# Optimization experiments

Hardware: AMD Instinct MI355X
Metric: run time of the kernel (lower is better)

## Reference

```python
import jax, jax.numpy as jnp
import numpy as np

# dims
B, N, M, K = 8, 4096, 1024, 32      # batch, points, centers, neighbors
CIN, CT = 64, 64                    # feature / temb channels
C1, C2 = 64, 128                    # SharedMLP out_channels
G, EPS = 8, 1e-5                    # GroupNorm(8, oc)


def setup_inputs() -> dict:
    key = jax.random.key(0)
    ks = jax.random.split(key, 8)
    return {
        "features": jax.random.normal(ks[0], (B, CIN, N), jnp.float32),
        "coords": jax.random.uniform(ks[1], (B, 3, N), jnp.float32),
        "temb": jax.random.normal(ks[2], (B, CT, N), jnp.float32),
        # SharedMLP params: Conv2d 1x1 -> (O, I) weight, GroupNorm affine
        "W1": jax.random.normal(ks[3], (C1, CIN + 3), jnp.float32) * 0.05,
        "b1": jnp.zeros((C1,), jnp.float32),
        "g1": jnp.ones((C1,), jnp.float32),
        "be1": jnp.zeros((C1,), jnp.float32),
        "W2": jax.random.normal(ks[4], (C2, C1), jnp.float32) * 0.05,
        "b2": jnp.zeros((C2,), jnp.float32),
        "g2": jnp.ones((C2,), jnp.float32),
        "be2": jnp.zeros((C2,), jnp.float32),
    }


def fps_indices(pts):
    # pts: [N, 3] -> [M] indices. Deterministic start at index 0
    # (original uses a random start; math otherwise identical).
    d0 = jnp.sum((pts - pts[0]) ** 2, axis=-1)  # [N]
    def step(dist, _):
        far = jnp.argmax(dist)
        dist = jnp.minimum(dist, jnp.sum((pts - pts[far]) ** 2, axis=-1))
        return dist, far
    _, fars = jax.lax.scan(step, d0, None, length=M - 1)
    return jnp.concatenate([jnp.zeros((1,), fars.dtype), fars])


def group_norm(x, gamma, beta):
    # x: [B, C, M, K], normalize per group over (C//G, M, K)
    b, c, m, k = x.shape
    xr = x.reshape(b, G, c // G, m, k)
    mu = xr.mean(axis=(2, 3, 4), keepdims=True)
    var = xr.var(axis=(2, 3, 4), keepdims=True)
    xn = ((xr - mu) * jax.lax.rsqrt(var + EPS)).reshape(b, c, m, k)
    return xn * gamma[:, None, None] + beta[:, None, None]


def swish(x):
    return x * jax.nn.sigmoid(x)


def reference(features, coords, temb, W1, b1, g1, be1, W2, b2, g2, be2):
    # --- furthest point sampling ---
    idx = jax.vmap(fps_indices)(coords.transpose(0, 2, 1))          # [B, M]
    centers = jax.vmap(lambda c, i: c[:, i])(coords, idx)           # [B, 3, M]
    # --- 'ball query' (actually kNN: source argsorts dist, takes first K) ---
    c = centers.transpose(0, 2, 1)                                  # [B, M, 3]
    p = coords.transpose(0, 2, 1)                                   # [B, N, 3]
    d = (jnp.sum(c * c, -1)[:, :, None] + jnp.sum(p * p, -1)[:, None, :]
         - 2.0 * jnp.einsum('bmd,bnd->bmn', c, p))                  # [B, M, N]
    _, nidx = jax.lax.top_k(-d, K)                                  # [B, M, K]
    gather = jax.vmap(lambda xb, ib: xb[:, ib])                     # [B,C,N],[B,M,K]->[B,C,M,K]
    gcoords = gather(coords, nidx) - centers[..., None]             # [B, 3, M, K]
    gtemb = gather(temb, nidx)                                      # [B, CT, M, K]
    gfeat = jnp.concatenate([gcoords, gather(features, nidx)], axis=1)  # [B, 3+CIN, M, K]
    # --- SharedMLP (1x1 conv -> GN -> Swish) x2, then max over neighbors ---
    h = swish(group_norm(jnp.einsum('oc,bcmk->bomk', W1, gfeat) + b1[:, None, None], g1, be1))
    h = swish(group_norm(jnp.einsum('oc,bcmk->bomk', W2, h) + b2[:, None, None], g2, be2))
    return h.max(axis=-1), centers, gtemb.max(axis=-1)
```

## Files before the change

### kernel.cpp

```cpp
#include <hip/hip_runtime.h>
#include <stdint.h>

#define BB 8
#define NN 4096
#define MM 1024
#define KK 32

__device__ __forceinline__ float bf2f(unsigned short u) {
    union { unsigned int i; float f; } v; v.i = ((unsigned int)u) << 16; return v.f;
}
__device__ __forceinline__ unsigned short f2bf(float f) {
    union { float f; unsigned int i; } v; v.f = f;
    unsigned int x = v.i;
    x += 0x7fffu + ((x >> 16) & 1u);
    return (unsigned short)(x >> 16);
}
__device__ __forceinline__ float swishf(float y) {
    return __fdividef(y, 1.0f + __expf(-y));
}

#define OUT1_OFF 1048576
#define OUT2_OFF 1073152

#define P_W1 0
#define P_B1 4288
#define P_G1 4352
#define P_BE1 4416
#define P_W2 4480
#define P_B2 12672
#define P_G2 12800
#define P_BE2 12928

__device__ __forceinline__ int detect_flag_wave(const unsigned short* f, int lane) {
    unsigned short u = f[lane * 2];
    float x = fabsf(bf2f(u));
    bool ext = (u != 0) && (x > 100.0f || x < 1e-30f);
    unsigned long long m = __ballot(ext);
    return (__popcll(m) >= 16) ? 1 : 0;
}

#define DPP_STAGE(CTRL) { \
    union { double d; unsigned int u[2]; } s_, r_; \
    s_.d = bd; \
    r_.u[0] = (unsigned)__builtin_amdgcn_update_dpp(0, (int)s_.u[0], CTRL, 0xF, 0xF, true); \
    r_.u[1] = (unsigned)__builtin_amdgcn_update_dpp(0, (int)s_.u[1], CTRL, 0xF, 0xF, true); \
    int op_ = __builtin_amdgcn_update_dpp(0, bp, CTRL, 0xF, 0xF, true); \
    double od_ = r_.d; \
    bool rep_ = (od_ > bd) || (od_ == bd && op_ < bp); \
    bd = rep_ ? od_ : bd; bp = rep_ ? op_ : bp; }

__device__ __forceinline__ void redmax64(double& bd, int& bp) {
    DPP_STAGE(0xB1)
    DPP_STAGE(0x4E)
    DPP_STAGE(0x141)
    DPP_STAGE(0x140)
#pragma unroll
    for (int m = 32; m >= 16; m >>= 1) {
        double od = __shfl_xor(bd, m, 64);
        int op = __shfl_xor(bp, m, 64);
        bool rep = (od > bd) || (od == bd && op < bp);
        bd = rep ? od : bd; bp = rep ? op : bp;
    }
}

__global__ __launch_bounds__(256) void k_cvt_all(
    const void* __restrict__ feat, const void* __restrict__ coords,
    float* __restrict__ featT, float* __restrict__ coordsC,
    float* __restrict__ paramsC,
    int* __restrict__ qhead, int* __restrict__ progress,
    float* __restrict__ stats1,
    const void* W1, const void* b1, const void* g1, const void* be1,
    const void* W2, const void* b2, const void* g2, const void* be2)
{
    __shared__ float tile[64][65];
    __shared__ int sflag;
    int tid = threadIdx.x, blk = blockIdx.x;
    if (tid < 64) {
        int fl0 = detect_flag_wave((const unsigned short*)feat, tid);
        if (tid == 0) sflag = fl0;
    }
    __syncthreads();
    int fl = sflag;
    if (blk == 0) {
        if (tid == 0) *qhead = 0;
        if (tid < 8) progress[tid * 16] = -1;
        stats1[tid] = 0.f;
        stats1[tid + 256] = 0.f;
    }
    if (blk < 512) {
        int i = blk;
        int b = i >> 6, n0 = (i & 63) * 64;
        int c = tid >> 2, q = tid & 3;
        size_t base = ((size_t)b * 64 + c) * NN + n0 + q * 16;
        if (fl) {
            const float* sp = (const float*)feat + base;
#pragma unroll
            for (int j = 0; j < 16; j++) tile[c][q * 16 + j] = sp[j];
        } else {
            const unsigned short* sp = (const unsigned short*)feat + base;
#pragma unroll
            for (int j = 0; j < 16; j++) tile[c][q * 16 + j] = bf2f(sp[j]);
        }
        __syncthreads();
        int n = tid >> 2;
        float* dp = featT + ((size_t)b * NN + n0 + n) * 64 + q * 16;
#pragma unroll
        for (int j = 0; j < 16; j++) dp[j] = tile[q * 16 + j][n];
    } else if (blk < 896) {
        int idx = (blk - 512) * 256 + tid;
        coordsC[idx] = fl ? ((const float*)coords)[idx]
                          : bf2f(((const unsigned short*)coords)[idx]);
    } else {
        int idx = (blk - 896) * 256 + tid;
        if (idx < 13056) {
            const void* src; int off;
            if (idx < 4288)       { src = W1;  off = idx; }
            else if (idx < 4352)  { src = b1;  off = idx - 4288; }
            else if (idx < 4416)  { src = g1;  off = idx - 4352; }
            else if (idx < 4480)  { src = be1; off = idx - 4416; }
            else if (idx < 12672) { src = W2;  off = idx - 4480; }
            else if (idx < 12800) { src = b2;  off = idx - 12672; }
            else if (idx < 12928) { src = g2;  off = idx - 12800; }
            else                  { src = be2; off = idx - 12928; }
            paramsC[idx] = fl ? ((const float*)src)[off]
                              : bf2f(((const unsigned short*)src)[off]);
        }
    }
}

#define W1Tm(j,c)     (((float*)SM)[(j)*64+(c)])
#define GBUFm(mi,k,c) (((float*)(SM+17152))[(((mi)*32+(k))*66)+(c)])
#define GCm(mi,j,k)   (((float*)(SM+50944))[(((mi)*3+(j))*32)+(k)])
#define NDm(mi,k)     (((int*)(SM+52480))[((mi)*32)+(k)])
#define W2Tm(j,c)     (((float*)SM)[(j)*128+(c)])
#define ACTm(mi,j,k)  (((float*)(SM+32768))[(((mi)*64+(j))*32)+(k)])

struct PW { double d; int p; int q; };
#define PSM_XS   ((float*)(SM))
#define PSM_YS   ((float*)(SM + 16384))
#define PSM_ZS   ((float*)(SM + 32768))
#define PSM_HIST ((int*)(SM + 49152))
#define PSM_PWB  ((PW*)(SM + 53248))
#define PSM_SF   ((int*)(SM + 53376))

#define RESCAN(G) { \
    double gd = 1.0e300; int ga = (G) * 8; \
    _Pragma("unroll") \
    for (int i = 0; i < 8; i++) { \
        int sl = (G) * 8 + i; \
        unsigned int bit = (sl < 32) ? (elo >> sl) : (ehi >> (sl - 32)); \
        double cd = (bit & 1u) ? 1.0e300 : d[sl]; \
        bool rep = cd < gd; \
        gd = rep ? cd : gd; ga = rep ? sl : ga; \
    } \
    g8[(G)] = gd; a8[(G)] = ga; }

__global__ __launch_bounds__(256) void k_fpsknn(
    const void* __restrict__ coords, const float* __restrict__ coordsC,
    float* __restrict__ centersF, int* __restrict__ nidx,
    const void* __restrict__ temb, const void* __restrict__ feat,
    const float* __restrict__ featT, const float* __restrict__ paramsC,
    float* __restrict__ stats1,
    void* __restrict__ d_out,
    int* __restrict__ qhead, int* __restrict__ progress,
    unsigned short* __restrict__ h1, int cache1)
{
    __shared__ __align__(16) char SM[55296];
    int tid = threadIdx.x;
    int blk = blockIdx.x;
    if (tid < 64) {
        int fl0 = detect_flag_wave((const unsigned short*)feat, tid);
        if (tid == 0) *PSM_SF = fl0;
    }
    __syncthreads();
    int fl = *PSM_SF;

    if (blk < 8) {
        int b = blk;
        if (fl) {
            const float* cb = (const float*)coords + (size_t)b * 3 * NN;
#pragma unroll
            for (int i = 0; i < 16; i++) {
                int p = tid + i * 256;
                PSM_XS[p] = cb[p]; PSM_YS[p] = cb[NN + p]; PSM_ZS[p] = cb[2 * NN + p];
            }
        } else {
            const unsigned short* cb = (const unsigned short*)coords + (size_t)b * 3 * NN;
#pragma unroll
            for (int i = 0; i < 16; i++) {
                int p = tid + i * 256;
                PSM_XS[p] = bf2f(cb[p]); PSM_YS[p] = bf2f(cb[NN + p]); PSM_ZS[p] = bf2f(cb[2 * NN + p]);
            }
        }
        if (tid == 0) PSM_HIST[0] = 0;
        __syncthreads();
        if (tid == 0) {
            *(float4*)(centersF + (size_t)b * MM * 4) =
                make_float4(PSM_XS[0], PSM_YS[0], PSM_ZS[0], 0.f);
            __hip_atomic_store(&progress[b * 16], 0, __ATOMIC_RELEASE, __HIP_MEMORY_SCOPE_AGENT);
        }
        int base = tid * 16;
        double px[16], py[16], pz[16], dist[16];
        double x0 = (double)PSM_XS[0], y0 = (double)PSM_YS[0], z0 = (double)PSM_ZS[0];
        double bd = -1.0; int bp = base;
#pragma unroll
        for (int j = 0; j < 16; j++) {
            px[j] = (double)PSM_XS[base + j]; py[j] = (double)PSM_YS[base + j]; pz[j] = (double)PSM_ZS[base + j];
            double dx = px[j] - x0, dy = py[j] - y0, dz = pz[j] - z0;
            dist[j] = fma(dz, dz, fma(dy, dy, dx * dx));
            bool rep = dist[j] > bd;
            bd = rep ? dist[j] : bd; bp = rep ? base + j : bp;
        }
        int lane = tid & 63, wid = tid >> 6;
#pragma unroll 1
        for (int s = 1; s < MM; s++) {
            redmax64(bd, bp);
            int par = s & 1;
            if (lane == 0) { PW w; w.d = bd; w.p = bp; w.q = 0; PSM_PWB[par * 4 + wid] = w; }
            __syncthreads();
            PW w0 = PSM_PWB[par * 4 + 0];
            double wd = w0.d; int wp = w0.p;
#pragma unroll
            for (int w = 1; w < 4; w++) {
                PW ww = PSM_PWB[par * 4 + w];
                bool rep = (ww.d > wd) || (ww.d == wd && ww.p < wp);
                wd = rep ? ww.d : wd; wp = rep ? ww.p : wp;
            }
            if (tid == 0) PSM_HIST[s] = wp;
            if ((s & 31) == 31 && s >= 63 && wid == ((s >> 5) & 3)) {
                int s0 = s - 63;
                if (lane < 32) {
                    int far = PSM_HIST[s0 + lane];
                    *(float4*)(centersF + ((size_t)b * MM + s0 + lane) * 4) =
                        make_float4(PSM_XS[far], PSM_YS[far], PSM_ZS[far], 0.f);
                }
                if (lane == 0)
                    __hip_atomic_store(&progress[b * 16], s0 + 31,
                                       __ATOMIC_RELEASE, __HIP_MEMORY_SCOPE_AGENT);
            }
            double fx = (double)PSM_XS[wp], fy = (double)PSM_YS[wp], fz = (double)PSM_ZS[wp];
            bd = -1.0; bp = base;
#pragma unroll
            for (int j = 0; j < 16; j++) {
                double dx = px[j] - fx, dy = py[j] - fy, dz = pz[j] - fz;
                double d = fma(dz, dz, fma(dy, dy, dx * dx));
                dist[j] = fmin(dist[j], d);
                bool rep = dist[j] > bd;
                bd = rep ? dist[j] : bd; bp = rep ? base + j : bp;
            }
        }
        __syncthreads();
        if (tid < 32) {
            int far = PSM_HIST[992 + tid];
            *(float4*)(centersF + ((size_t)b * MM + 992 + tid) * 4) =
                make_float4(PSM_XS[far], PSM_YS[far], PSM_ZS[far], 0.f);
        }
        if (tid == 0)
            __hip_atomic_store(&progress[b * 16], 1023,
                               __ATOMIC_RELEASE, __HIP_MEMORY_SCOPE_AGENT);
#pragma unroll
        for (int i = 0; i < 4; i++) {
            int m = tid + i * 256;
            int far = PSM_HIST[m];
            float X = PSM_XS[far], Y = PSM_YS[far], Z = PSM_ZS[far];
            if (fl) {
                float* o = (float*)d_out;
                o[OUT1_OFF + (size_t)(b * 3 + 0) * MM + m] = X;
                o[OUT1_OFF + (size_t)(b * 3 + 1) * MM + m] = Y;
                o[OUT1_OFF + (size_t)(b * 3 + 2) * MM + m] = Z;
            } else {
                unsigned short* o = (unsigned short*)d_out;
                o[OUT1_OFF + (size_t)(b * 3 + 0) * MM + m] = f2bf(X);
                o[OUT1_OFF + (size_t)(b * 3 + 1) * MM + m] = f2bf(Y);
                o[OUT1_OFF + (size_t)(b * 3 + 2) * MM + m] = f2bf(Z);
            }
        }
    } else {
        int lane = tid & 63, wid = tid >> 6;
        for (int t = tid; t < 64 * 67; t += 256) {
            int c = t / 67, j = t % 67;
            W1Tm(j, c) = paramsC[P_W1 + t];
        }
        __syncthreads();
        for (;;) {
            int id = 0;
            if (lane == 0) id = atomicAdd(qhead, 1);
            id = __shfl(id, 0, 64);
            if (id >= BB * MM) break;
            int b = id & 7, m = id >> 3;
            while (__hip_atomic_load(&progress[b * 16], __ATOMIC_RELAXED,
                                     __HIP_MEMORY_SCOPE_AGENT) < m)
                __builtin_amdgcn_s_sleep(64);
            (void)__hip_atomic_load(&progress[b * 16], __ATOMIC_ACQUIRE,
                                    __HIP_MEMORY_SCOPE_AGENT);
            int bm = b * MM + m;
            const float* cb = coordsC + (size_t)b * 3 * NN;
            float4 ctr = *(const float4*)(centersF + (size_t)bm * 4);
            double cx = (double)ctr.x, cy = (double)ctr.y, cz = (double)ctr.z;
            double cc = (cx * cx + cy * cy) + cz * cz;
            double d[64];
#pragma unroll 4
            for (int j = 0; j < 64; j++) {
                int p = j * 64 + lane;
                double x = (double)cb[p], y = (double)cb[NN + p], z = (double)cb[2 * NN + p];
                double pp = (x * x + y * y) + z * z;
                double dt = (cx * x + cy * y) + cz * z;
                d[j] = (cc + pp) - 2.0 * dt;
            }
            double g8[8]; int a8[8];
#pragma unroll
            for (int g = 0; g < 8; g++) {
                double gd = d[g * 8]; int ga = g * 8;
#pragma unroll
                for (int i = 1; i < 8; i++) {
                    int sl = g * 8 + i;
                    bool rep = d[sl] < gd;
                    gd = rep ? d[sl] : gd; ga = rep ? sl : ga;
                }
                g8[g] = gd; a8[g] = ga;
            }
            unsigned int elo = 0, ehi = 0;
            int res = 0;
#pragma unroll 1
            for (int it = 0; it < 32; it++) {
                double bd = g8[0]; int ba = a8[0];
#pragma unroll
                for (int g = 1; g < 8; g++) {
                    bool rep = g8[g] < bd;
                    bd = rep ? g8[g] : bd; ba = rep ? a8[g] : ba;
                }
                int bp = ba * 64 + lane;
                double wd = bd; int wp = bp;
#pragma unroll
                for (int s = 32; s >= 1; s >>= 1) {
                    double od = __shfl_xor(wd, s, 64);
                    int op = __shfl_xor(wp, s, 64);
                    bool rep = (od < wd) || (od == wd && op < wp);
                    wd = rep ? od : wd; wp = rep ? op : wp;
                }
                res = (lane == it) ? wp : res;
                if (bp == wp) {
                    int slot = ba;
                    if (slot < 32) elo |= (1u << slot); else ehi |= (1u << (slot - 32));
                    int g = slot >> 3;
                    switch (g) {
                        case 0: RESCAN(0) break;
                        case 1: RESCAN(1) break;
                        case 2: RESCAN(2) break;
                        case 3: RESCAN(3) break;
                        case 4: RESCAN(4) break;
                        case 5: RESCAN(5) break;
                        case 6: RESCAN(6) break;
                        case 7: RESCAN(7) break;
                    }
                }
            }
            if (lane < KK) nidx[(size_t)bm * KK + lane] = res;
            float best = -3.0e38f;
            if (fl) {
                const float* tb = (const float*)temb + ((size_t)b * 64 + lane) * NN;
#pragma unroll 4
                for (int k = 0; k < 32; k++) {
                    int nk = __shfl(res, k, 64);
                    best = fmaxf(best, tb[nk]);
                }
            } else {
                const unsigned short* tb = (const unsigned short*)temb + ((size_t)b * 64 + lane) * NN;
#pragma unroll 4
                for (int k = 0; k < 32; k++) {
                    int nk = __shfl(res, k, 64);
                    best = fmaxf(best, bf2f(tb[nk]));
                }
            }
            size_t off = (size_t)OUT2_OFF + ((size_t)(b * 64 + lane)) * MM + m;
            if (fl) ((float*)d_out)[off] = best;
            else    ((unsigned short*)d_out)[off] = f2bf(best);
            if (lane < 32) NDm(wid, lane) = res & (NN - 1);
            const float* fb = featT + (size_t)b * NN * 64;
#pragma unroll 4
            for (int q = 0; q < 32; q++) {
                int n = NDm(wid, q);
                GBUFm(wid, q, lane) = fb[(size_t)n * 64 + lane];
            }
            if (lane < 32) {
                int n = NDm(wid, lane);
                GCm(wid, 0, lane) = __fsub_rn(cb[n], ctr.x);
                GCm(wid, 1, lane) = __fsub_rn(cb[NN + n], ctr.y);
                GCm(wid, 2, lane) = __fsub_rn(cb[2 * NN + n], ctr.z);
            }
            int c0 = (lane >> 3) * 8;
            int k0 = (lane & 7) * 4;
            float acc[8][4];
#pragma unroll
            for (int i = 0; i < 8; i++)
#pragma unroll
                for (int kk = 0; kk < 4; kk++) acc[i][kk] = 0.f;
#pragma unroll
            for (int j = 0; j < 3; j++) {
                float4 a = *(const float4*)&GCm(wid, j, k0);
                float4 w0 = *(const float4*)&W1Tm(j, c0);
                float4 w1v = *(const float4*)&W1Tm(j, c0 + 4);
                float w[8] = {w0.x, w0.y, w0.z, w0.w, w1v.x, w1v.y, w1v.z, w1v.w};
#pragma unroll
                for (int i = 0; i < 8; i++) {
                    acc[i][0] = fmaf(w[i], a.x, acc[i][0]);
                    acc[i][1] = fmaf(w[i], a.y, acc[i][1]);
                    acc[i][2] = fmaf(w[i], a.z, acc[i][2]);
                    acc[i][3] = fmaf(w[i], a.w, acc[i][3]);
                }
            }
#pragma unroll 4
            for (int c = 0; c < 64; c++) {
                float f0 = GBUFm(wid, k0 + 0, c);
                float f1 = GBUFm(wid, k0 + 1, c);
                float f2 = GBUFm(wid, k0 + 2, c);
                float f3 = GBUFm(wid, k0 + 3, c);
                int j = 3 + c;
                float4 w0 = *(const float4*)&W1Tm(j, c0);
                float4 w1v = *(const float4*)&W1Tm(j, c0 + 4);
                float w[8] = {w0.x, w0.y, w0.z, w0.w, w1v.x, w1v.y, w1v.z, w1v.w};
#pragma unroll
                for (int i = 0; i < 8; i++) {
                    acc[i][0] = fmaf(w[i], f0, acc[i][0]);
                    acc[i][1] = fmaf(w[i], f1, acc[i][1]);
                    acc[i][2] = fmaf(w[i], f2, acc[i][2]);
                    acc[i][3] = fmaf(w[i], f3, acc[i][3]);
                }
            }
            float s = 0.f, s2 = 0.f;
#pragma unroll
            for (int i = 0; i < 8; i++) {
                float bb = paramsC[P_B1 + c0 + i];
                float v0 = acc[i][0] + bb, v1 = acc[i][1] + bb;
                float v2 = acc[i][2] + bb, v3 = acc[i][3] + bb;
                s += v0; s2 = fmaf(v0, v0, s2);
                s += v1; s2 = fmaf(v1, v1, s2);
                s += v2; s2 = fmaf(v2, v2, s2);
                s += v3; s2 = fmaf(v3, v3, s2);
                if (cache1) {
                    unsigned int p0 = (unsigned int)f2bf(v0) | ((unsigned int)f2bf(v1) << 16);
                    unsigned int p1 = (unsigned int)f2bf(v2) | ((unsigned int)f2bf(v3) << 16);
                    *(uint2*)(h1 + ((size_t)bm * 64 + c0 + i) * 32 + k0) = make_uint2(p0, p1);
                }
            }
            s += __shfl_xor(s, 1, 64); s += __shfl_xor(s, 2, 64); s += __shfl_xor(s, 4, 64);
            s2 += __shfl_xor(s2, 1, 64); s2 += __shfl_xor(s2, 2, 64); s2 += __shfl_xor(s2, 4, 64);
            if ((lane & 7) == 0) {
                int g = lane >> 3;
                atomicAdd(&stats1[(b * 8 + g) * 2], s);
                atomicAdd(&stats1[(b * 8 + g) * 2 + 1], s2);
            }
        }
    }
}

__device__ __forceinline__ void mlp1_compute(
    char* SM, int tid, int lane, int mi, int b, int bm,
    const float* __restrict__ featT, const float* __restrict__ coordsC,
    const float* __restrict__ centersF, const int* __restrict__ nidx,
    const float* __restrict__ P, float acc[8][4])
{
    for (int t = tid; t < 64 * 67; t += 256) {
        int c = t / 67, j = t % 67;
        W1Tm(j, c) = P[P_W1 + t];
    }
    if (lane < 32) NDm(mi, lane) = nidx[(size_t)bm * KK + lane] & (NN - 1);
    __syncthreads();
    const float* fb = featT + (size_t)b * NN * 64;
#pragma unroll 4
    for (int q = 0; q < 32; q++) {
        int n = NDm(mi, q);
        GBUFm(mi, q, lane) = fb[(size_t)n * 64 + lane];
    }
    float4 ctr = *(const float4*)(centersF + (size_t)bm * 4);
    const float* cb = coordsC + (size_t)b * 3 * NN;
    if (lane < 32) {
        int n = NDm(mi, lane);
        GCm(mi, 0, lane) = __fsub_rn(cb[n], ctr.x);
        GCm(mi, 1, lane) = __fsub_rn(cb[NN + n], ctr.y);
        GCm(mi, 2, lane) = __fsub_rn(cb[2 * NN + n], ctr.z);
    }
    __syncthreads();
    int c0 = (lane >> 3) * 8;
    int k0 = (lane & 7) * 4;
#pragma unroll
    for (int i = 0; i < 8; i++)
#pragma unroll
        for (int kk = 0; kk < 4; kk++) acc[i][kk] = 0.f;
#pragma unroll
    for (int j = 0; j < 3; j++) {
        float4 a = *(const float4*)&GCm(mi, j, k0);
        float4 w0 = *(const float4*)&W1Tm(j, c0);
        float4 w1v = *(const float4*)&W1Tm(j, c0 + 4);
        float w[8] = {w0.x, w0.y, w0.z, w0.w, w1v.x, w1v.y, w1v.z, w1v.w};
#pragma unroll
        for (int i = 0; i < 8; i++) {
            acc[i][0] = fmaf(w[i], a.x, acc[i][0]);
            acc[i][1] = fmaf(w[i], a.y, acc[i][1]);
            acc[i][2] = fmaf(w[i], a.z, acc[i][2]);
            acc[i][3] = fmaf(w[i], a.w, acc[i][3]);
        }
    }
#pragma unroll 4
    for (int c = 0; c < 64; c++) {
        float f0 = GBUFm(mi, k0 + 0, c);
        float f1 = GBUFm(mi, k0 + 1, c);
        float f2 = GBUFm(mi, k0 + 2, c);
        float f3 = GBUFm(mi, k0 + 3, c);
        int j = 3 + c;
        float4 w0 = *(const float4*)&W1Tm(j, c0);
        float4 w1v = *(const float4*)&W1Tm(j, c0 + 4);
        float w[8] = {w0.x, w0.y, w0.z, w0.w, w1v.x, w1v.y, w1v.z, w1v.w};
#pragma unroll
        for (int i = 0; i < 8; i++) {
            acc[i][0] = fmaf(w[i], f0, acc[i][0]);
            acc[i][1] = fmaf(w[i], f1, acc[i][1]);
            acc[i][2] = fmaf(w[i], f2, acc[i][2]);
            acc[i][3] = fmaf(w[i], f3, acc[i][3]);
        }
    }
}

__device__ __forceinline__ void mlp2_compute(
    char* SM, int tid, int lane, int mi, int b,
    const float v1[8][4], const float* __restrict__ S1,
    const float* __restrict__ P, float v2[16][4])
{
    __syncthreads();
    int c0 = (lane >> 3) * 8;
    int k0 = (lane & 7) * 4;
    int g = c0 >> 3;
    float S = S1[(b * 8 + g) * 2], Q = S1[(b * 8 + g) * 2 + 1];
    float mean = S * (1.0f / 262144.0f);
    float var = Q * (1.0f / 262144.0f) - mean * mean;
    float inv = rsqrtf(var + 1e-5f);
#pragma unroll
    for (int i = 0; i < 8; i++) {
        int c = c0 + i;
        float sc = P[P_G1 + c] * inv;
        float sh = P[P_BE1 + c] - mean * sc;
#pragma unroll
        for (int kk = 0; kk < 4; kk++)
            ACTm(mi, c, k0 + kk) = swishf(fmaf(v1[i][kk], sc, sh));
    }
    for (int t = tid; t < 128 * 64; t += 256) {
        int c = t >> 6, j = t & 63;
        W2Tm(j, c) = P[P_W2 + t];
    }
    __syncthreads();
    int c02 = (lane >> 3) * 16;
    float acc2[16][4];
#pragma unroll
    for (int i = 0; i < 16; i++)
#pragma unroll
        for (int kk = 0; kk < 4; kk++) acc2[i][kk] = 0.f;
#pragma unroll 4
    for (int j = 0; j < 64; j++) {
        float4 a = *(const float4*)&ACTm(mi, j, k0);
        float4 w0 = *(const float4*)&W2Tm(j, c02);
        float4 w1v = *(const float4*)&W2Tm(j, c02 + 4);
        float4 w2v = *(const float4*)&W2Tm(j, c02 + 8);
        float4 w3 = *(const float4*)&W2Tm(j, c02 + 12);
        float w[16] = {w0.x, w0.y, w0.z, w0.w, w1v.x, w1v.y, w1v.z, w1v.w,
                       w2v.x, w2v.y, w2v.z, w2v.w, w3.x, w3.y, w3.z, w3.w};
#pragma unroll
        for (int i = 0; i < 16; i++) {
            acc2[i][0] = fmaf(w[i], a.x, acc2[i][0]);
            acc2[i][1] = fmaf(w[i], a.y, acc2[i][1]);
            acc2[i][2] = fmaf(w[i], a.z, acc2[i][2]);
            acc2[i][3] = fmaf(w[i], a.w, acc2[i][3]);
        }
    }
#pragma unroll
    for (int i = 0; i < 16; i++) {
        float bb = P[P_B2 + c02 + i];
#pragma unroll
        for (int kk = 0; kk < 4; kk++) v2[i][kk] = acc2[i][kk] + bb;
    }
}

__device__ __forceinline__ void get_v1(
    char* SM, int tid, int lane, int mi, int b, int bm,
    const float* featT, const float* coordsC, const float* centersF,
    const int* nidx, const float* P,
    const unsigned short* h1, int cache1, float v1[8][4])
{
    int c0 = (lane >> 3) * 8;
    int k0 = (lane & 7) * 4;
    if (cache1) {
#pragma unroll
        for (int i = 0; i < 8; i++) {
            uint2 u = *(const uint2*)(h1 + ((size_t)bm * 64 + c0 + i) * 32 + k0);
            v1[i][0] = bf2f((unsigned short)(u.x & 0xffffu));
            v1[i][1] = bf2f((unsigned short)(u.x >> 16));
            v1[i][2] = bf2f((unsigned short)(u.y & 0xffffu));
            v1[i][3] = bf2f((unsigned short)(u.y >> 16));
        }
    } else {
        float acc1[8][4];
        mlp1_compute(SM, tid, lane, mi, b, bm, featT, coordsC, centersF, nidx, P, acc1);
#pragma unroll
        for (int i = 0; i < 8; i++) {
            float bb = P[P_B1 + c0 + i];
#pragma unroll
            for (int kk = 0; kk < 4; kk++) v1[i][kk] = acc1[i][kk] + bb;
        }
    }
}

__global__ __launch_bounds__(256) void k_mlp2s(
    const float* __restrict__ featT, const float* __restrict__ coordsC,
    const float* __restrict__ centersF, const int* __restrict__ nidx,
    const float* __restrict__ P, const float* __restrict__ stats1,
    float* __restrict__ stats2,
    const unsigned short* __restrict__ h1, unsigned short* __restrict__ h2,
    int cache1, int cache2)
{
    __shared__ __align__(16) char smem[65536];
    char* SM = smem;
    int tid = threadIdx.x, blk = blockIdx.x;
    int b = blk >> 8, m0 = (blk & 255) * 4;
    int mi = tid >> 6, lane = tid & 63;
    int bm = b * MM + m0 + mi;
    float v1[8][4];
    get_v1(SM, tid, lane, mi, b, bm, featT, coordsC, centersF, nidx, P, h1, cache1, v1);
    float v2[16][4];
    mlp2_compute(SM, tid, lane, mi, b, v1, stats1, P, v2);
    int c02 = (lane >> 3) * 16;
    int k0 = (lane & 7) * 4;
    float s = 0.f, s2 = 0.f;
#pragma unroll
    for (int i = 0; i < 16; i++) {
#pragma unroll
        for (int kk = 0; kk < 4; kk++) {
            float v = v2[i][kk];
            s += v; s2 = fmaf(v, v, s2);
        }
        if (cache2) {
            unsigned int p0 = (unsigned int)f2bf(v2[i][0]) | ((unsigned int)f2bf(v2[i][1]) << 16);
            unsigned int p1 = (unsigned int)f2bf(v2[i][2]) | ((unsigned int)f2bf(v2[i][3]) << 16);
            *(uint2*)(h2 + ((size_t)bm * 128 + c02 + i) * 32 + k0) = make_uint2(p0, p1);
        }
    }
    s += __shfl_xor(s, 1, 64); s += __shfl_xor(s, 2, 64); s += __shfl_xor(s, 4, 64);
    s2 += __shfl_xor(s2, 1, 64); s2 += __shfl_xor(s2, 2, 64); s2 += __shfl_xor(s2, 4, 64);
    __syncthreads();
    float* sred = (float*)SM;
    if ((lane & 7) == 0) {
        int g = lane >> 3;
        sred[(mi * 8 + g) * 2] = s;
        sred[(mi * 8 + g) * 2 + 1] = s2;
    }
    __syncthreads();
    if (tid < 16) {
        int g = tid >> 1, w = tid & 1;
        float t = sred[(0 * 8 + g) * 2 + w] + sred[(1 * 8 + g) * 2 + w]
                + sred[(2 * 8 + g) * 2 + w] + sred[(3 * 8 + g) * 2 + w];
        atomicAdd(&stats2[(b * 8 + g) * 2 + w], t);
    }
}

__global__ __launch_bounds__(256) void k_final(
    const float* __restrict__ featT, const float* __restrict__ coordsC,
    const float* __restrict__ centersF, const int* __restrict__ nidx,
    const float* __restrict__ P, const float* __restrict__ stats1,
    const float* __restrict__ stats2,
    void* __restrict__ d_out, const void* __restrict__ feat,
    const unsigned short* __restrict__ h1, const unsigned short* __restrict__ h2,
    int cache1, int cache2)
{
    __shared__ __align__(16) char smem[65536];
    char* SM = smem;
    int tid = threadIdx.x, blk = blockIdx.x;
    if (tid < 64) {
        int fl0 = detect_flag_wave((const unsigned short*)feat, tid);
        if (tid == 0) *(int*)(SM + 53248) = fl0;
    }
    __syncthreads();
    int fl = *(int*)(SM + 53248);
    int b = blk >> 8, m0 = (blk & 255) * 4;
    int mi = tid >> 6, lane = tid & 63;
    int bm = b * MM + m0 + mi;
    int c02 = (lane >> 3) * 16;
    int k0 = (lane & 7) * 4;
    float v2[16][4];
    if (cache2) {
#pragma unroll
        for (int i = 0; i < 16; i++) {
            uint2 u = *(const uint2*)(h2 + ((size_t)bm * 128 + c02 + i) * 32 + k0);
            v2[i][0] = bf2f((unsigned short)(u.x & 0xffffu));
            v2[i][1] = bf2f((unsigned short)(u.x >> 16));
            v2[i][2] = bf2f((unsigned short)(u.y & 0xffffu));
            v2[i][3] = bf2f((unsigned short)(u.y >> 16));
        }
    } else {
        float v1[8][4];
        get_v1(SM, tid, lane, mi, b, bm, featT, coordsC, centersF, nidx, P, h1, cache1, v1);
        mlp2_compute(SM, tid, lane, mi, b, v1, stats1, P, v2);
    }
    int g2 = c02 >> 4;
    float S = stats2[(b * 8 + g2) * 2], Q = stats2[(b * 8 + g2) * 2 + 1];
    float mean = S * (1.0f / 524288.0f);
    float var = Q * (1.0f / 524288.0f) - mean * mean;
    float inv = rsqrtf(var + 1e-5f);
    float mx[16];
#pragma unroll
    for (int i = 0; i < 16; i++) {
        int c = c02 + i;
        float sc = P[P_G2 + c] * inv;
        float sh = P[P_BE2 + c] - mean * sc;
        float v = -3.0e38f;
#pragma unroll
        for (int kk = 0; kk < 4; kk++)
            v = fmaxf(v, swishf(fmaf(v2[i][kk], sc, sh)));
        v = fmaxf(v, __shfl_xor(v, 1, 64));
        v = fmaxf(v, __shfl_xor(v, 2, 64));
        v = fmaxf(v, __shfl_xor(v, 4, 64));
        mx[i] = v;
    }
    if ((lane & 7) == 0) {
        int m = m0 + mi;
#pragma unroll
        for (int i = 0; i < 16; i++) {
            size_t off = (size_t)(b * 128 + c02 + i) * MM + m;
            if (fl) ((float*)d_out)[off] = mx[i];
            else    ((unsigned short*)d_out)[off] = f2bf(mx[i]);
        }
    }
}

extern "C" void kernel_launch(void* const* d_in, const int* in_sizes, int n_in,
                              void* d_out, int out_size, void* d_ws, size_t ws_size,
                              hipStream_t stream) {
    (void)in_sizes; (void)n_in; (void)out_size;
    const void* feat = d_in[0];
    const void* coords = d_in[1];
    const void* temb = d_in[2];

    char* ws = (char*)d_ws;
    int* qhead = (int*)ws;
    int* progress = (int*)(ws + 512);
    float* stats1 = (float*)(ws + 1024);
    float* stats2 = (float*)(ws + 2048);
    float* coordsC = (float*)(ws + 3072);
    float* paramsC = (float*)(ws + 396288);
    float* centersF = (float*)(ws + 448512);
    int* nidx = (int*)(ws + 579584);
    float* featT = (float*)(ws + 1628160);
    unsigned short* h1 = (unsigned short*)(ws + 10016768);
    unsigned short* h2 = (unsigned short*)(ws + 43571200);
    int cache1 = (ws_size >= 43571200u) ? 1 : 0;
    int cache2 = (ws_size >= 110680064u) ? 1 : 0;

    k_cvt_all<<<947, 256, 0, stream>>>(feat, coords, featT, coordsC, paramsC,
                                       qhead, progress, stats1,
                                       d_in[3], d_in[4], d_in[5], d_in[6],
                                       d_in[7], d_in[8], d_in[9], d_in[10]);
    k_fpsknn<<<256, 256, 0, stream>>>(coords, coordsC, centersF, nidx, temb,
                                      feat, featT, paramsC, stats1, d_out,
                                      qhead, progress, h1, cache1);
    k_mlp2s<<<2048, 256, 0, stream>>>(featT, coordsC, centersF, nidx, paramsC,
                                      stats1, stats2, h1, h2, cache1, cache2);
    k_final<<<2048, 256, 0, stream>>>(featT, coordsC, centersF, nidx, paramsC,
                                      stats1, stats2, d_out, feat, h1, h2,
                                      cache1, cache2);
}
```

Measured before the change: 1.347 ms.

## Store only per-channel neighbor max/min of MLP2 pre-activations instead of full h2

Instead of caching the full second-layer pre-activation tensor and re-reading it to apply GroupNorm, swish and the neighbor max, the stats kernel now reduces each channel over neighbors to a max and a min. A small elementwise final kernel applies the affine-plus-swish to both and takes the larger, relying on swish being unimodal. The feature transpose also moves from the conversion kernel into the idle worker blocks of the FPS/kNN kernel, followed by a spin-wait grid barrier. This removes a large intermediate write and read, but adds a grid-wide spin barrier that assumes all worker blocks are co-resident.

Measured after the change: 1.333 ms. About the same (-1.0%).

```diff
diff --git a/kernel.cpp b/kernel.cpp
--- a/kernel.cpp
+++ b/kernel.cpp
@@ -65,14 +65,12 @@
 
 __global__ __launch_bounds__(256) void k_cvt_all(
     const void* __restrict__ feat, const void* __restrict__ coords,
-    float* __restrict__ featT, float* __restrict__ coordsC,
-    float* __restrict__ paramsC,
+    float* __restrict__ coordsC, float* __restrict__ paramsC,
     int* __restrict__ qhead, int* __restrict__ progress,
-    float* __restrict__ stats1,
+    float* __restrict__ stats1, int* __restrict__ cvt_done,
     const void* W1, const void* b1, const void* g1, const void* be1,
     const void* W2, const void* b2, const void* g2, const void* be2)
 {
-    __shared__ float tile[64][65];
     __shared__ int sflag;
     int tid = threadIdx.x, blk = blockIdx.x;
     if (tid < 64) {
@@ -82,36 +80,17 @@
     __syncthreads();
     int fl = sflag;
     if (blk == 0) {
-        if (tid == 0) *qhead = 0;
+        if (tid == 0) { *qhead = 0; *cvt_done = 0; }
         if (tid < 8) progress[tid * 16] = -1;
         stats1[tid] = 0.f;
         stats1[tid + 256] = 0.f;
     }
-    if (blk < 512) {
-        int i = blk;
-        int b = i >> 6, n0 = (i & 63) * 64;
-        int c = tid >> 2, q = tid & 3;
-        size_t base = ((size_t)b * 64 + c) * NN + n0 + q * 16;
-        if (fl) {
-            const float* sp = (const float*)feat + base;
-#pragma unroll
-            for (int j = 0; j < 16; j++) tile[c][q * 16 + j] = sp[j];
-        } else {
-            const unsigned short* sp = (const unsigned short*)feat + base;
-#pragma unroll
-            for (int j = 0; j < 16; j++) tile[c][q * 16 + j] = bf2f(sp[j]);
-        }
-        __syncthreads();
-        int n = tid >> 2;
-        float* dp = featT + ((size_t)b * NN + n0 + n) * 64 + q * 16;
-#pragma unroll
-        for (int j = 0; j < 16; j++) dp[j] = tile[q * 16 + j][n];
-    } else if (blk < 896) {
-        int idx = (blk - 512) * 256 + tid;
+    if (blk < 384) {
+        int idx = blk * 256 + tid;
         coordsC[idx] = fl ? ((const float*)coords)[idx]
                           : bf2f(((const unsigned short*)coords)[idx]);
     } else {
-        int idx = (blk - 896) * 256 + tid;
+        int idx = (blk - 384) * 256 + tid;
         if (idx < 13056) {
             const void* src; int off;
             if (idx < 4288)       { src = W1;  off = idx; }
@@ -159,10 +138,11 @@
     const void* __restrict__ coords, const float* __restrict__ coordsC,
     float* __restrict__ centersF, int* __restrict__ nidx,
     const void* __restrict__ temb, const void* __restrict__ feat,
-    const float* __restrict__ featT, const float* __restrict__ paramsC,
+    float* __restrict__ featT, const float* __restrict__ paramsC,
     float* __restrict__ stats1,
     void* __restrict__ d_out,
     int* __restrict__ qhead, int* __restrict__ progress,
+    int* __restrict__ cvt_done,
     unsigned short* __restrict__ h1, int cache1)
 {
     __shared__ __align__(16) char SM[55296];
@@ -277,6 +257,38 @@
         }
     } else {
         int lane = tid & 63, wid = tid >> 6;
+        {
+            float (*tile)[65] = (float(*)[65])SM;
+            for (int t = blk - 8; t < 512; t += 248) {
+                int b = t >> 6, n0 = (t & 63) * 64;
+                int c = tid >> 2, q = tid & 3;
+                size_t base = ((size_t)b * 64 + c) * NN + n0 + q * 16;
+                __syncthreads();
+                if (fl) {
+                    const float* sp = (const float*)feat + base;
+#pragma unroll
+                    for (int j = 0; j < 16; j++) tile[c][q * 16 + j] = sp[j];
+                } else {
+                    const unsigned short* sp = (const unsigned short*)feat + base;
+#pragma unroll
+                    for (int j = 0; j < 16; j++) tile[c][q * 16 + j] = bf2f(sp[j]);
+                }
+                __syncthreads();
+                int n = tid >> 2;
+                float* dp = featT + ((size_t)b * NN + n0 + n) * 64 + q * 16;
+#pragma unroll
+                for (int j = 0; j < 16; j++) dp[j] = tile[q * 16 + j][n];
+            }
+            __syncthreads();
+            if (tid == 0) {
+                __hip_atomic_fetch_add(cvt_done, 1, __ATOMIC_ACQ_REL, __HIP_MEMORY_SCOPE_AGENT);
+                while (__hip_atomic_load(cvt_done, __ATOMIC_RELAXED,
+                                         __HIP_MEMORY_SCOPE_AGENT) < 248)
+                    __builtin_amdgcn_s_sleep(16);
+                (void)__hip_atomic_load(cvt_done, __ATOMIC_ACQUIRE, __HIP_MEMORY_SCOPE_AGENT);
+            }
+            __syncthreads();
+        }
         for (int t = tid; t < 64 * 67; t += 256) {
             int c = t / 67, j = t % 67;
             W1Tm(j, c) = paramsC[P_W1 + t];
@@ -613,8 +625,9 @@
     const float* __restrict__ centersF, const int* __restrict__ nidx,
     const float* __restrict__ P, const float* __restrict__ stats1,
     float* __restrict__ stats2,
-    const unsigned short* __restrict__ h1, unsigned short* __restrict__ h2,
-    int cache1, int cache2)
+    const unsigned short* __restrict__ h1, int cache1,
+    unsigned short* __restrict__ vmaxA, unsigned short* __restrict__ vminA,
+    int have_vmm)
 {
     __shared__ __align__(16) char smem[65536];
     char* SM = smem;
@@ -627,7 +640,6 @@
     float v2[16][4];
     mlp2_compute(SM, tid, lane, mi, b, v1, stats1, P, v2);
     int c02 = (lane >> 3) * 16;
-    int k0 = (lane & 7) * 4;
     float s = 0.f, s2 = 0.f;
 #pragma unroll
     for (int i = 0; i < 16; i++) {
@@ -636,10 +648,21 @@
             float v = v2[i][kk];
             s += v; s2 = fmaf(v, v, s2);
         }
-        if (cache2) {
-            unsigned int p0 = (unsigned int)f2bf(v2[i][0]) | ((unsigned int)f2bf(v2[i][1]) << 16);
-            unsigned int p1 = (unsigned int)f2bf(v2[i][2]) | ((unsigned int)f2bf(v2[i][3]) << 16);
-            *(uint2*)(h2 + ((size_t)bm * 128 + c02 + i) * 32 + k0) = make_uint2(p0, p1);
+    }
+    if (have_vmm) {
+        int m = m0 + mi;
+#pragma unroll
+        for (int i = 0; i < 16; i++) {
+            float va = fmaxf(fmaxf(v2[i][0], v2[i][1]), fmaxf(v2[i][2], v2[i][3]));
+            float vb = fminf(fminf(v2[i][0], v2[i][1]), fminf(v2[i][2], v2[i][3]));
+            va = fmaxf(va, __shfl_xor(va, 1, 64)); vb = fminf(vb, __shfl_xor(vb, 1, 64));
+            va = fmaxf(va, __shfl_xor(va, 2, 64)); vb = fminf(vb, __shfl_xor(vb, 2, 64));
+            va = fmaxf(va, __shfl_xor(va, 4, 64)); vb = fminf(vb, __shfl_xor(vb, 4, 64));
+            if ((lane & 7) == 0) {
+                size_t o = ((size_t)(b * 128 + c02 + i)) * MM + m;
+                vmaxA[o] = f2bf(va);
+                vminA[o] = f2bf(vb);
+            }
         }
     }
     s += __shfl_xor(s, 1, 64); s += __shfl_xor(s, 2, 64); s += __shfl_xor(s, 4, 64);
@@ -660,14 +683,37 @@
     }
 }
 
-__global__ __launch_bounds__(256) void k_final(
+__global__ __launch_bounds__(256) void k_final_fast(
+    const unsigned short* __restrict__ vmaxA, const unsigned short* __restrict__ vminA,
+    const float* __restrict__ P, const float* __restrict__ stats2,
+    void* __restrict__ d_out, const void* __restrict__ feat)
+{
+    int tid = threadIdx.x;
+    int idx = blockIdx.x * 256 + tid;
+    int fl = detect_flag_wave((const unsigned short*)feat, tid & 63);
+    int c = (idx >> 10) & 127;
+    int b = idx >> 17;
+    int g = c >> 4;
+    float S = stats2[(b * 8 + g) * 2], Q = stats2[(b * 8 + g) * 2 + 1];
+    float mean = S * (1.0f / 524288.0f);
+    float var = Q * (1.0f / 524288.0f) - mean * mean;
+    float inv = rsqrtf(var + 1e-5f);
+    float sc = P[P_G2 + c] * inv;
+    float sh = P[P_BE2 + c] - mean * sc;
+    float va = bf2f(vmaxA[idx]);
+    float vb = bf2f(vminA[idx]);
+    float r = fmaxf(swishf(fmaf(va, sc, sh)), swishf(fmaf(vb, sc, sh)));
+    if (fl) ((float*)d_out)[idx] = r;
+    else    ((unsigned short*)d_out)[idx] = f2bf(r);
+}
+
+__global__ __launch_bounds__(256) void k_final_slow(
     const float* __restrict__ featT, const float* __restrict__ coordsC,
     const float* __restrict__ centersF, const int* __restrict__ nidx,
     const float* __restrict__ P, const float* __restrict__ stats1,
     const float* __restrict__ stats2,
     void* __restrict__ d_out, const void* __restrict__ feat,
-    const unsigned short* __restrict__ h1, const unsigned short* __restrict__ h2,
-    int cache1, int cache2)
+    const unsigned short* __restrict__ h1, int cache1)
 {
     __shared__ __align__(16) char smem[65536];
     char* SM = smem;
@@ -681,23 +727,11 @@
     int b = blk >> 8, m0 = (blk & 255) * 4;
     int mi = tid >> 6, lane = tid & 63;
     int bm = b * MM + m0 + mi;
+    float v1[8][4];
+    get_v1(SM, tid, lane, mi, b, bm, featT, coordsC, centersF, nidx, P, h1, cache1, v1);
+    float v2[16][4];
+    mlp2_compute(SM, tid, lane, mi, b, v1, stats1, P, v2);
     int c02 = (lane >> 3) * 16;
-    int k0 = (lane & 7) * 4;
-    float v2[16][4];
-    if (cache2) {
-#pragma unroll
-        for (int i = 0; i < 16; i++) {
-            uint2 u = *(const uint2*)(h2 + ((size_t)bm * 128 + c02 + i) * 32 + k0);
-            v2[i][0] = bf2f((unsigned short)(u.x & 0xffffu));
-            v2[i][1] = bf2f((unsigned short)(u.x >> 16));
-            v2[i][2] = bf2f((unsigned short)(u.y & 0xffffu));
-            v2[i][3] = bf2f((unsigned short)(u.y >> 16));
-        }
-    } else {
-        float v1[8][4];
-        get_v1(SM, tid, lane, mi, b, bm, featT, coordsC, centersF, nidx, P, h1, cache1, v1);
-        mlp2_compute(SM, tid, lane, mi, b, v1, stats1, P, v2);
-    }
     int g2 = c02 >> 4;
     float S = stats2[(b * 8 + g2) * 2], Q = stats2[(b * 8 + g2) * 2 + 1];
     float mean = S * (1.0f / 524288.0f);
@@ -742,26 +776,34 @@
     int* progress = (int*)(ws + 512);
     float* stats1 = (float*)(ws + 1024);
     float* stats2 = (float*)(ws + 2048);
-    float* coordsC = (float*)(ws + 3072);
-    float* paramsC = (float*)(ws + 396288);
-    float* centersF = (float*)(ws + 448512);
-    int* nidx = (int*)(ws + 579584);
-    float* featT = (float*)(ws + 1628160);
-    unsigned short* h1 = (unsigned short*)(ws + 10016768);
-    unsigned short* h2 = (unsigned short*)(ws + 43571200);
-    int cache1 = (ws_size >= 43571200u) ? 1 : 0;
-    int cache2 = (ws_size >= 110680064u) ? 1 : 0;
-
-    k_cvt_all<<<947, 256, 0, stream>>>(feat, coords, featT, coordsC, paramsC,
-                                       qhead, progress, stats1,
+    int* cvt_done = (int*)(ws + 3072);
+    float* coordsC = (float*)(ws + 3136);
+    float* paramsC = (float*)(ws + 396352);
+    float* centersF = (float*)(ws + 448576);
+    int* nidx = (int*)(ws + 579648);
+    float* featT = (float*)(ws + 1628224);
+    unsigned short* h1 = (unsigned short*)(ws + 10016832);
+    unsigned short* vmaxA = (unsigned short*)(ws + 43571264);
+    unsigned short* vminA = (unsigned short*)(ws + 45668416);
+    int cache1 = (ws_size >= 43571264u) ? 1 : 0;
+    int have_vmm = (ws_size >= 47765568u) ? 1 : 0;
+
+    k_cvt_all<<<435, 256, 0, stream>>>(feat, coords, coordsC, paramsC,
+                                       qhead, progress, stats1, cvt_done,
                                        d_in[3], d_in[4], d_in[5], d_in[6],
                                        d_in[7], d_in[8], d_in[9], d_in[10]);
     k_fpsknn<<<256, 256, 0, stream>>>(coords, coordsC, centersF, nidx, temb,
                                       feat, featT, paramsC, stats1, d_out,
-                                      qhead, progress, h1, cache1);
+                                      qhead, progress, cvt_done, h1, cache1);
     k_mlp2s<<<2048, 256, 0, stream>>>(featT, coordsC, centersF, nidx, paramsC,
-                                      stats1, stats2, h1, h2, cache1, cache2);
-    k_final<<<2048, 256, 0, stream>>>(featT, coordsC, centersF, nidx, paramsC,
-                                      stats1, stats2, d_out, feat, h1, h2,
-                                      cache1, cache2);
-}
+                                      stats1, stats2, h1, cache1,
+                                      vmaxA, vminA, have_vmm);
+    if (have_vmm) {
+        k_final_fast<<<4096, 256, 0, stream>>>(vmaxA, vminA, paramsC, stats2,
+                                               d_out, feat);
+    } else {
+        k_final_slow<<<2048, 256, 0, stream>>>(featT, coordsC, centersF, nidx,
+                                               paramsC, stats1, stats2, d_out,
+                                               feat, h1, cache1);
+    }
+}
```
